# Performance work log

Measured on AMD Instinct MI355X. Metric: run time of the kernel, lower is better.

Reference implementation:

```python
import jax, jax.numpy as jnp
import numpy as np

N_HEAD = 32
D_MODEL = 4096
N_KV_GROUPS = 8
D_HEAD = D_MODEL // N_HEAD            # 128
H_PER_G = N_HEAD // N_KV_GROUPS       # 4
KV_DIM = N_KV_GROUPS * D_HEAD         # 1024
B, S = 2, 2048


def setup_inputs() -> dict:
    key = jax.random.key(0)
    ks = jax.random.split(key, 8)
    q = jax.random.normal(ks[0], (B, S, D_MODEL), dtype=jnp.float32)
    k = jax.random.normal(ks[1], (B, S, D_MODEL), dtype=jnp.float32)
    v = jax.random.normal(ks[2], (B, S, D_MODEL), dtype=jnp.float32)
    # causal mask (True = keep), broadcast over b, g, h as in the torch module
    mask = jnp.tril(jnp.ones((S, S), dtype=bool))
    # params: torch init is torch.rand (uniform [0,1)); scale down for numerics
    w_q = jax.random.uniform(ks[3], (D_MODEL, D_MODEL), dtype=jnp.float32) * 0.02
    w_k = jax.random.uniform(ks[4], (KV_DIM, D_MODEL), dtype=jnp.float32) * 0.02
    w_v = jax.random.uniform(ks[5], (KV_DIM, D_MODEL), dtype=jnp.float32) * 0.02
    w_out = jax.random.uniform(ks[6], (D_MODEL, D_MODEL), dtype=jnp.float32) * 0.02
    return {"q": q, "k": k, "v": v, "w_q": w_q, "w_k": w_k, "w_v": w_v,
            "w_out": w_out, "mask": mask}


def reference(q, k, v, w_q, w_k, w_v, w_out, mask):
    b, n, _ = q.shape
    s = k.shape[1]
    # F.linear(x, W) == x @ W.T
    query = q @ w_q.T                                  # [b, n, d_model]
    key = k @ w_k.T                                    # [b, s, kv_dim]
    value = v @ w_v.T                                  # [b, s, kv_dim]
    # b n (h d) -> b h n d -> b g h n d
    query = query.reshape(b, n, N_HEAD, D_HEAD).transpose(0, 2, 1, 3)
    query = query.reshape(b, N_KV_GROUPS, H_PER_G, n, D_HEAD)
    # b s (g d) -> b g s d
    key = key.reshape(b, s, N_KV_GROUPS, D_HEAD).transpose(0, 2, 1, 3)
    value = value.reshape(b, s, N_KV_GROUPS, D_HEAD).transpose(0, 2, 1, 3)
    scores = jnp.einsum('bghnd,bgsd->bghns', query, key) / (D_HEAD ** 0.5)
    scores = jnp.where(mask, scores, jnp.finfo(scores.dtype).min)
    attention = jax.nn.softmax(scores, axis=-1)        # [b, g, h, n, s]
    out = jnp.einsum('bghns,bgsd->bghnd', attention, value)
    # b g h n d -> b n (g h d)
    out = out.transpose(0, 3, 1, 2, 4).reshape(b, n, D_MODEL)
    return out @ w_out.T
```

## Files before the change

### kernel.cpp

```cpp
#include <hip/hip_runtime.h>

typedef unsigned short u16;
typedef unsigned int u32;
typedef __bf16 bf16x8 __attribute__((ext_vector_type(8)));
typedef float f32x4 __attribute__((ext_vector_type(4)));
typedef u16 u16x8 __attribute__((ext_vector_type(8)));
typedef u32 u32x2 __attribute__((ext_vector_type(2)));

#define SCL2E 0.12751744898229718f

__device__ __forceinline__ u16 f2bf(float f) {
  union { float f; u32 u; } x; x.f = f;
  u32 r = x.u + 0x7fffu + ((x.u >> 16) & 1u);
  return (u16)(r >> 16);
}

__device__ __forceinline__ u32 cvt_pk_bf16(float lo, float hi) {
  u32 r;
  asm("v_cvt_pk_bf16_f32 %0, %1, %2" : "=v"(r) : "v"(lo), "v"(hi));
  return r;
}

__device__ __forceinline__ void gld16(const void* g, void* l) {
  __builtin_amdgcn_global_load_lds(
      (const __attribute__((address_space(1))) u32*)g,
      (__attribute__((address_space(3))) u32*)l, 16, 0, 0);
}

#define SBAR() __builtin_amdgcn_s_barrier()
#define WAITVM(N) do { asm volatile("s_waitcnt vmcnt(" #N ")" ::: "memory"); \
                       __builtin_amdgcn_sched_barrier(0); } while (0)

#define STG(G, R0, DST, RIT, KT, K) do { \
    int rit_ = (RIT) + w*8 + lr; \
    int ch_ = lch ^ (rit_ & 7); \
    gld16((G) + ((R0) + rit_) * (long)(K) + (long)(KT)*64 + ch_*8, \
          (DST) + ((RIT) + w*8)*64); } while (0)

__device__ __forceinline__ void cvt_body(const float* __restrict__ in,
                                         u16* __restrict__ out, int n8) {
  int stride = gridDim.x * 256;
  for (int i = blockIdx.x * 256 + threadIdx.x; i < n8; i += stride) {
    float4 a = ((const float4*)in)[2*i];
    float4 b = ((const float4*)in)[2*i+1];
    u16x8 o;
    o[0]=f2bf(a.x); o[1]=f2bf(a.y); o[2]=f2bf(a.z); o[3]=f2bf(a.w);
    o[4]=f2bf(b.x); o[5]=f2bf(b.y); o[6]=f2bf(b.z); o[7]=f2bf(b.w);
    ((u16x8*)out)[i] = o;
  }
}

__global__ __launch_bounds__(256) void cvt3(
    const float* __restrict__ i0, const float* __restrict__ i1,
    const float* __restrict__ i2, u16* __restrict__ o0,
    u16* __restrict__ o1, u16* __restrict__ o2, int n8) {
  const float* in = blockIdx.y == 0 ? i0 : (blockIdx.y == 1 ? i1 : i2);
  u16* out = blockIdx.y == 0 ? o0 : (blockIdx.y == 1 ? o1 : o2);
  cvt_body(in, out, n8);
}

#define MFMA_(A, B, C) __builtin_amdgcn_mfma_f32_16x16x32_bf16(A, B, C, 0, 0, 0)

template<int OUTF32>
__device__ __forceinline__ void gemm256_body(
    const u16* __restrict__ Ag, const u16* __restrict__ Bg, void* __restrict__ Cp,
    const int K, const int ldc, const long m0, const long n0, const long cb,
    const float escale, u16* __restrict__ As, u16* __restrict__ Bs) {
  const int lane = threadIdx.x & 63, w = threadIdx.x >> 6;
  const int wm = w >> 2, wn = w & 3;
  const int c = lane & 15, grp = lane >> 4;
  const int lr = lane >> 3, lch = lane & 7;

  f32x4 acc[8][4] = {};
  const int NK = K >> 6;

  STG(Bg, n0, Bs, 0, 0, K);   STG(Bg, n0, Bs, 64, 0, K);
  STG(Bg, n0, Bs, 128, 0, K); STG(Bg, n0, Bs, 192, 0, K);
  STG(Ag, m0, As, 0, 0, K);   STG(Ag, m0, As, 128, 0, K);
  STG(Ag, m0, As, 64, 0, K);  STG(Ag, m0, As, 192, 0, K);
  {
    u16* B1 = Bs + 16384;
    STG(Bg, n0, B1, 0, 1, K);   STG(Bg, n0, B1, 64, 1, K);
    STG(Bg, n0, B1, 128, 1, K); STG(Bg, n0, B1, 192, 1, K);
  }
  WAITVM(6);
  SBAR();

  for (int kt = 0; kt < NK; ++kt) {
    const u16* At = As + (kt & 1) * 16384;
    u16* An = As + ((kt & 1) ^ 1) * 16384;
    const u16* Bt = Bs + (kt % 3) * 16384;
    u16* Bn = Bs + ((kt + 2) % 3) * 16384;
    const bool am = (kt + 1 < NK), bm = (kt + 2 < NK);

    bf16x8 bfr[4];
#define LDAF(mi, ks) (*(const bf16x8*)(At + (wm*128 + (mi)*16 + c)*64 + ((((ks)*4 + grp)) ^ (c & 7))*8))
#define LDBF(ni, ks) (*(const bf16x8*)(Bt + (wn*64  + (ni)*16 + c)*64 + ((((ks)*4 + grp)) ^ (c & 7))*8))
#define BLD(KS) bfr[0] = LDBF(0, KS); bfr[1] = LDBF(1, KS); \
                bfr[2] = LDBF(2, KS); bfr[3] = LDBF(3, KS);

#define PHASE4(MB, KS, BLOADS, STAGES, WAITS) { \
    bf16x8 a0 = LDAF((MB)+0, KS), a1 = LDAF((MB)+1, KS); \
    bf16x8 a2 = LDAF((MB)+2, KS), a3 = LDAF((MB)+3, KS); \
    BLOADS \
    STAGES \
    WAITS \
    SBAR(); \
    __builtin_amdgcn_s_setprio(1); \
    _Pragma("unroll") \
    for (int ni = 0; ni < 4; ++ni) { \
      acc[(MB)+0][ni] = MFMA_(a0, bfr[ni], acc[(MB)+0][ni]); \
      acc[(MB)+1][ni] = MFMA_(a1, bfr[ni], acc[(MB)+1][ni]); \
      acc[(MB)+2][ni] = MFMA_(a2, bfr[ni], acc[(MB)+2][ni]); \
      acc[(MB)+3][ni] = MFMA_(a3, bfr[ni], acc[(MB)+3][ni]); \
    } \
    __builtin_amdgcn_s_setprio(0); \
    SBAR(); }

    PHASE4(0, 0, BLD(0),
           if (am) { STG(Ag, m0, An, 0, kt+1, K); STG(Ag, m0, An, 128, kt+1, K); },
           if (am) { WAITVM(6); } else { WAITVM(0); })
    PHASE4(4, 0, ;,
           if (am) { STG(Ag, m0, An, 64, kt+1, K); STG(Ag, m0, An, 192, kt+1, K); }, ;)
    PHASE4(0, 1, BLD(1),
           if (bm) { STG(Bg, n0, Bn, 0, kt+2, K); STG(Bg, n0, Bn, 64, kt+2, K); }, ;)
    PHASE4(4, 1, ;,
           if (bm) { STG(Bg, n0, Bn, 128, kt+2, K); STG(Bg, n0, Bn, 192, kt+2, K); WAITVM(6); }
           else if (am) { WAITVM(2); }, ;)
#undef PHASE4
#undef BLD
#undef LDAF
#undef LDBF
  }

  #pragma unroll
  for (int mi = 0; mi < 8; ++mi) {
    #pragma unroll
    for (int rr = 0; rr < 4; ++rr) {
      long row = m0 + wm*128 + mi*16 + grp*4 + rr;
      #pragma unroll
      for (int ni = 0; ni < 4; ++ni) {
        long col = cb + wn*64 + ni*16 + c;
        if (OUTF32) ((float*)Cp)[row*ldc + col] = acc[mi][ni][rr];
        else        ((u16*)Cp)[row*ldc + col]  = f2bf(acc[mi][ni][rr] * escale);
      }
    }
  }
}

__device__ __forceinline__ void gemm128_body(
    const u16* __restrict__ Ag, const u16* __restrict__ Bg, u16* __restrict__ Cp,
    const int K, const int ldc, const long m0, const long n0, const long cb,
    u16* __restrict__ As, u16* __restrict__ Bs) {
  const int lane = threadIdx.x & 63, w = threadIdx.x >> 6;
  const int wm = w >> 2, wn = w & 3;
  const int c = lane & 15, grp = lane >> 4;
  const int lr = lane >> 3, lch = lane & 7;

  f32x4 acc[4][4] = {};
  const int NK = K >> 6;

  STG(Bg, n0, Bs, 0, 0, K);   STG(Bg, n0, Bs, 64, 0, K);
  STG(Bg, n0, Bs, 128, 0, K); STG(Bg, n0, Bs, 192, 0, K);
  STG(Ag, m0, As, 0, 0, K);   STG(Ag, m0, As, 64, 0, K);
  {
    u16* B1 = Bs + 16384; u16* A1 = As + 8192;
    STG(Bg, n0, B1, 0, 1, K);   STG(Bg, n0, B1, 64, 1, K);
    STG(Bg, n0, B1, 128, 1, K); STG(Bg, n0, B1, 192, 1, K);
    STG(Ag, m0, A1, 0, 1, K);   STG(Ag, m0, A1, 64, 1, K);
  }
  WAITVM(6);
  SBAR();

  for (int kt = 0; kt < NK; ++kt) {
    const u16* At = As + (kt % 3) * 8192;
    const u16* Bt = Bs + (kt % 3) * 16384;
    u16* An = As + ((kt + 2) % 3) * 8192;
    u16* Bn = Bs + ((kt + 2) % 3) * 16384;
    const bool bm = (kt + 2 < NK);

    bf16x8 bfr[4];
#define LDAF(mi, ks) (*(const bf16x8*)(At + (wm*64 + (mi)*16 + c)*64 + ((((ks)*4 + grp)) ^ (c & 7))*8))
#define LDBF(ni, ks) (*(const bf16x8*)(Bt + (wn*64 + (ni)*16 + c)*64 + ((((ks)*4 + grp)) ^ (c & 7))*8))

#define PHASE2K(KS, STAGES, WAITS) { \
    bf16x8 a0 = LDAF(0, KS), a1 = LDAF(1, KS); \
    bf16x8 a2 = LDAF(2, KS), a3 = LDAF(3, KS); \
    bfr[0] = LDBF(0, KS); bfr[1] = LDBF(1, KS); \
    bfr[2] = LDBF(2, KS); bfr[3] = LDBF(3, KS); \
    STAGES \
    WAITS \
    SBAR(); \
    __builtin_amdgcn_s_setprio(1); \
    _Pragma("unroll") \
    for (int ni = 0; ni < 4; ++ni) { \
      acc[0][ni] = MFMA_(a0, bfr[ni], acc[0][ni]); \
      acc[1][ni] = MFMA_(a1, bfr[ni], acc[1][ni]); \
      acc[2][ni] = MFMA_(a2, bfr[ni], acc[2][ni]); \
      acc[3][ni] = MFMA_(a3, bfr[ni], acc[3][ni]); \
    } \
    __builtin_amdgcn_s_setprio(0); \
    SBAR(); }

    PHASE2K(0, if (bm) { STG(Bg, n0, Bn, 0, kt+2, K); STG(Bg, n0, Bn, 64, kt+2, K); }, ;)
    PHASE2K(1, if (bm) { STG(Bg, n0, Bn, 128, kt+2, K); STG(Bg, n0, Bn, 192, kt+2, K);
                         STG(Ag, m0, An, 0, kt+2, K); STG(Ag, m0, An, 64, kt+2, K); },
               if (bm) { WAITVM(6); } else { WAITVM(0); })
#undef PHASE2K
#undef LDAF
#undef LDBF
  }

  #pragma unroll
  for (int mi = 0; mi < 4; ++mi) {
    #pragma unroll
    for (int rr = 0; rr < 4; ++rr) {
      long row = m0 + wm*64 + mi*16 + grp*4 + rr;
      #pragma unroll
      for (int ni = 0; ni < 4; ++ni) {
        long col = cb + wn*64 + ni*16 + c;
        Cp[row*ldc + col] = f2bf(acc[mi][ni][rr]);
      }
    }
  }
}

__global__ __launch_bounds__(512, 2) void proj_gemm(
    const u16* __restrict__ qb, const u16* __restrict__ kb,
    const u16* __restrict__ vb, const u16* __restrict__ wqb,
    const u16* __restrict__ wkv, u16* __restrict__ Qp, u16* __restrict__ KVp) {
  __shared__ __attribute__((aligned(16))) u16 SMEM[81920];
  int wg = ((int)blockIdx.x & 7) * 32 + ((int)blockIdx.x >> 3);
  gemm256_body<0>(qb, wqb, Qp, 4096, 4096,
                  (long)(wg >> 4) * 256, (long)(wg & 15) * 256, (long)(wg & 15) * 256,
                  SCL2E, SMEM, SMEM + 32768);
  {
    int mt = wg >> 3, nt = wg & 7;
    const u16* A_ = (nt < 4) ? kb : vb;
    const u16* B_ = wkv + ((nt < 4) ? 0 : 4194304);
    long n0 = (long)(nt & 3) * 256;
    long cb = (nt < 4) ? n0 : n0 + 1024;
    gemm128_body(A_, B_, KVp, 4096, 2048, (long)mt * 128, n0, cb,
                 SMEM, SMEM + 24576);
  }
}

__global__ __launch_bounds__(512, 2) void gemm_out(
    const u16* __restrict__ A, const u16* __restrict__ Bw, float* __restrict__ C) {
  __shared__ __attribute__((aligned(16))) u16 SMEM[81920];
  int wg = ((int)blockIdx.x & 7) * 32 + ((int)blockIdx.x >> 3);
  long m0 = (long)(wg >> 4) * 256, n0 = (long)(wg & 15) * 256;
  gemm256_body<1>(A, Bw, C, 4096, 4096, m0, n0, n0, 1.f, SMEM, SMEM + 32768);
}

__global__ __launch_bounds__(256) void transpose_v(
    const u16* __restrict__ KVp, u16* __restrict__ Vt) {
  const int s0 = blockIdx.x * 64, n0 = blockIdx.y * 64, b = blockIdx.z;
  const int tid = threadIdx.x;
  __shared__ __attribute__((aligned(16))) u16 t[64*80];
  #pragma unroll
  for (int p = 0; p < 2; ++p) {
    int sl = p*32 + (tid >> 3), nl = (tid & 7) * 8;
    *(u16x8*)(t + sl*80 + nl) =
        *(const u16x8*)(KVp + (long)(b*2048 + s0 + sl)*2048 + 1024 + n0 + nl);
  }
  __syncthreads();
  #pragma unroll
  for (int p = 0; p < 2; ++p) {
    int nl = p*32 + (tid >> 3), sc = (tid & 7) * 8;
    u16x8 o;
    #pragma unroll
    for (int j = 0; j < 8; ++j) o[j] = t[(sc + j)*80 + nl];
    *(u16x8*)(Vt + (long)(b*1024 + n0 + nl)*2048 + s0 + sc) = o;
  }
}

__global__ __launch_bounds__(512, 2) void attn_fwd(
    const u16* __restrict__ Qp, const u16* __restrict__ KVp,
    const u16* __restrict__ Vt, u16* __restrict__ AO) {
  const int head = blockIdx.y, b = blockIdx.z;
  const int g = head >> 2;
  const int tid = threadIdx.x, lane = tid & 63, w = tid >> 6;
  const int c = lane & 15, grp = lane >> 4;

  __shared__ __attribute__((aligned(16))) u16 Ks[2][64*128];
  __shared__ __attribute__((aligned(16))) u16 Vts[2][128*64];
  __shared__ __attribute__((aligned(16))) u16 Ps[8][32*64];
  u16* __restrict__ pw = &Ps[w][0];

  for (int half = 0; half < 2; ++half) {
    const int qt = half ? (7 - (int)blockIdx.x) : (int)blockIdx.x;
    const int q0 = qt * 256;
    const int qw = q0 + w * 32;

    bf16x8 qf[2][4];
    #pragma unroll
    for (int h = 0; h < 2; ++h) {
      const u16* qb = Qp + (long)(b*2048 + qw + h*16 + c)*4096 + head*128 + grp*8;
      #pragma unroll
      for (int t = 0; t < 4; ++t) qf[h][t] = *(const bf16x8*)(qb + t*32);
    }

    float m_run[2] = {-1e30f, -1e30f}, l_run[2] = {0.f, 0.f};
    f32x4 oacc[2][8] = {};

    const int ntiles = 4*qt + 4;

    auto STAGE = [&](int buf, int kt) {
      const int kv0 = kt * 64;
      #pragma unroll
      for (int p = 0; p < 2; ++p) {
        int idx = p*512 + w*64 + lane;
        int krow = idx >> 4, kc = idx & 15;
        int kcs = kc ^ (krow & 7);
        gld16(KVp + (long)(b*2048 + kv0 + krow)*2048 + g*128 + kcs*8,
              &Ks[buf][(p*512 + w*64)*8]);
        int d = idx >> 3, vc = idx & 7;
        int vcs = vc ^ (d & 7);
        gld16(Vt + (long)(b*1024 + g*128 + d)*2048 + kv0 + vcs*8,
              &Vts[buf][(p*512 + w*64)*8]);
      }
    };

    if (half) __syncthreads();
    STAGE(0, 0);
    int cur = 0;
    for (int kt = 0; kt < ntiles; ++kt) {
      const int kv0 = kt * 64;
      __syncthreads();
      if (kt + 1 < ntiles) STAGE(cur ^ 1, kt + 1);

      if (kv0 <= qw + 31) {
        const u16* __restrict__ Kc = &Ks[cur][0];
        const u16* __restrict__ Vc = &Vts[cur][0];

        f32x4 sacc[2][4] = {};
        __builtin_amdgcn_s_setprio(1);
        #pragma unroll
        for (int f = 0; f < 4; ++f) {
          const int row = f*16 + c;
          #pragma unroll
          for (int t = 0; t < 4; ++t) {
            bf16x8 kf = *(const bf16x8*)(Kc + row*128 + (((t*4 + grp) ^ (c & 7)) * 8));
            sacc[0][f] = __builtin_amdgcn_mfma_f32_16x16x32_bf16(kf, qf[0][t], sacc[0][f], 0, 0, 0);
            sacc[1][f] = __builtin_amdgcn_mfma_f32_16x16x32_bf16(kf, qf[1][t], sacc[1][f], 0, 0, 0);
          }
        }
        __builtin_amdgcn_s_setprio(0);

        #pragma unroll
        for (int h = 0; h < 2; ++h) {
          const int qg = qw + h*16 + c;
          float sv[16];
          if (kv0 + 63 > qw + h*16) {
            #pragma unroll
            for (int f = 0; f < 4; ++f)
              #pragma unroll
              for (int r = 0; r < 4; ++r) {
                float x = sacc[h][f][r];
                if (kv0 + f*16 + grp*4 + r > qg) x = -1e30f;
                sv[f*4 + r] = x;
              }
          } else {
            #pragma unroll
            for (int f = 0; f < 4; ++f)
              #pragma unroll
              for (int r = 0; r < 4; ++r) sv[f*4 + r] = sacc[h][f][r];
          }
          float tm[8];
          #pragma unroll
          for (int i = 0; i < 8; ++i) tm[i] = fmaxf(sv[i], sv[i+8]);
          #pragma unroll
          for (int i = 0; i < 4; ++i) tm[i] = fmaxf(tm[i], tm[i+4]);
          float tmax = fmaxf(fmaxf(tm[0], tm[2]), fmaxf(tm[1], tm[3]));
          tmax = fmaxf(tmax, __shfl_xor(tmax, 16));
          tmax = fmaxf(tmax, __shfl_xor(tmax, 32));

          float m_new = m_run[h];
          if (!__all(tmax <= m_run[h] + 8.f)) {
            m_new = fmaxf(m_run[h], tmax);
            float corr = exp2f(m_run[h] - m_new);
            l_run[h] *= corr;
            #pragma unroll
            for (int n = 0; n < 8; ++n) oacc[h][n] *= corr;
            m_run[h] = m_new;
          }

          float tsum = 0.f;
          u32 pk[8];
          #pragma unroll
          for (int i = 0; i < 8; ++i) {
            float p0 = exp2f(sv[2*i]   - m_new);
            float p1 = exp2f(sv[2*i+1] - m_new);
            tsum += p0 + p1;
            pk[i] = cvt_pk_bf16(p0, p1);
          }
          tsum += __shfl_xor(tsum, 16);
          tsum += __shfl_xor(tsum, 32);
          l_run[h] += tsum;

          #pragma unroll
          for (int f = 0; f < 4; ++f) {
            int col = (f*16 + grp*4) ^ ((c & 7) << 3);
            u32x2 pv; pv[0] = pk[2*f]; pv[1] = pk[2*f + 1];
            *(u32x2*)(pw + (h*16 + c)*64 + col) = pv;
          }
        }

        __builtin_amdgcn_s_setprio(1);
        #pragma unroll
        for (int u = 0; u < 2; ++u) {
          const int pcol = (u*32 + grp*8) ^ ((c & 7) << 3);
          bf16x8 pf0 = *(const bf16x8*)(pw + c*64 + pcol);
          bf16x8 pf1 = *(const bf16x8*)(pw + (16 + c)*64 + pcol);
          #pragma unroll
          for (int n = 0; n < 8; ++n) {
            bf16x8 vf = *(const bf16x8*)(Vc + (n*16 + c)*64 + (((u*4 + grp) ^ (c & 7)) * 8));
            oacc[0][n] = __builtin_amdgcn_mfma_f32_16x16x32_bf16(vf, pf0, oacc[0][n], 0, 0, 0);
            oacc[1][n] = __builtin_amdgcn_mfma_f32_16x16x32_bf16(vf, pf1, oacc[1][n], 0, 0, 0);
          }
        }
        __builtin_amdgcn_s_setprio(0);
      }
      cur ^= 1;
    }

    #pragma unroll
    for (int h = 0; h < 2; ++h) {
      const float inv = 1.0f / l_run[h];
      u16* ob = AO + (long)(b*2048 + qw + h*16 + c)*4096 + head*128 + grp*4;
      #pragma unroll
      for (int n = 0; n < 8; ++n) {
        u32x2 o;
        o[0] = cvt_pk_bf16(oacc[h][n][0]*inv, oacc[h][n][1]*inv);
        o[1] = cvt_pk_bf16(oacc[h][n][2]*inv, oacc[h][n][3]*inv);
        *(u32x2*)(ob + n*16) = o;
      }
    }
  }
}

extern "C" void kernel_launch(void* const* d_in, const int* in_sizes, int n_in,
                              void* d_out, int out_size, void* d_ws, size_t ws_size,
                              hipStream_t stream) {
  const float* q   = (const float*)d_in[0];
  const float* k   = (const float*)d_in[1];
  const float* v   = (const float*)d_in[2];
  const float* w_q = (const float*)d_in[3];
  const float* w_k = (const float*)d_in[4];
  const float* w_v = (const float*)d_in[5];
  const float* w_o = (const float*)d_in[6];

  u16* ws  = (u16*)d_ws;
  u16* qb  = ws;
  u16* kb  = qb  + 16777216;
  u16* vb  = kb  + 16777216;
  u16* wqb = vb  + 16777216;
  u16* wob = wqb + 16777216;
  u16* wkv = wob + 16777216;
  u16* Qp  = wkv + 8388608;
  u16* KVp = Qp  + 16777216;
  u16* Vtr = kb;
  u16* AO  = vb;
  (void)ws_size; (void)in_sizes; (void)n_in; (void)out_size;

  dim3 blk(256);
  cvt3<<<dim3(2048,3), blk, 0, stream>>>(q, k, v, qb, kb, vb, 2097152);
  cvt3<<<dim3(2048,2), blk, 0, stream>>>(w_q, w_o, w_o, wqb, wob, wob, 2097152);
  cvt3<<<dim3(512, 2), blk, 0, stream>>>(w_k, w_v, w_v, wkv, wkv + 4194304, wkv + 4194304, 524288);

  proj_gemm<<<256, dim3(512), 0, stream>>>(qb, kb, vb, wqb, wkv, Qp, KVp);
  transpose_v<<<dim3(32,16,2), blk, 0, stream>>>(KVp, Vtr);
  attn_fwd<<<dim3(4,32,2), dim3(512), 0, stream>>>(Qp, KVp, Vtr, AO);
  gemm_out<<<256, dim3(512), 0, stream>>>(AO, wob, (float*)d_out);
}
```

Before: 537.0 us.

## Collapse per-phase barriers into one barrier per k-tile in GEMM main loops

```diff
diff --git a/kernel.cpp b/kernel.cpp
--- a/kernel.cpp
+++ b/kernel.cpp
@@ -28,6 +28,7 @@
 }
 
 #define SBAR() __builtin_amdgcn_s_barrier()
+#define SCHEDB() __builtin_amdgcn_sched_barrier(0)
 #define WAITVM(N) do { asm volatile("s_waitcnt vmcnt(" #N ")" ::: "memory"); \
                        __builtin_amdgcn_sched_barrier(0); } while (0)
 
@@ -76,14 +77,14 @@
 
   STG(Bg, n0, Bs, 0, 0, K);   STG(Bg, n0, Bs, 64, 0, K);
   STG(Bg, n0, Bs, 128, 0, K); STG(Bg, n0, Bs, 192, 0, K);
-  STG(Ag, m0, As, 0, 0, K);   STG(Ag, m0, As, 128, 0, K);
-  STG(Ag, m0, As, 64, 0, K);  STG(Ag, m0, As, 192, 0, K);
+  STG(Ag, m0, As, 0, 0, K);   STG(Ag, m0, As, 64, 0, K);
+  STG(Ag, m0, As, 128, 0, K); STG(Ag, m0, As, 192, 0, K);
   {
     u16* B1 = Bs + 16384;
     STG(Bg, n0, B1, 0, 1, K);   STG(Bg, n0, B1, 64, 1, K);
     STG(Bg, n0, B1, 128, 1, K); STG(Bg, n0, B1, 192, 1, K);
   }
-  WAITVM(6);
+  WAITVM(4);
   SBAR();
 
   for (int kt = 0; kt < NK; ++kt) {
@@ -93,19 +94,10 @@
     u16* Bn = Bs + ((kt + 2) % 3) * 16384;
     const bool am = (kt + 1 < NK), bm = (kt + 2 < NK);
 
-    bf16x8 bfr[4];
+    bf16x8 a0, a1, a2, a3, bfr[4];
 #define LDAF(mi, ks) (*(const bf16x8*)(At + (wm*128 + (mi)*16 + c)*64 + ((((ks)*4 + grp)) ^ (c & 7))*8))
 #define LDBF(ni, ks) (*(const bf16x8*)(Bt + (wn*64  + (ni)*16 + c)*64 + ((((ks)*4 + grp)) ^ (c & 7))*8))
-#define BLD(KS) bfr[0] = LDBF(0, KS); bfr[1] = LDBF(1, KS); \
-                bfr[2] = LDBF(2, KS); bfr[3] = LDBF(3, KS);
-
-#define PHASE4(MB, KS, BLOADS, STAGES, WAITS) { \
-    bf16x8 a0 = LDAF((MB)+0, KS), a1 = LDAF((MB)+1, KS); \
-    bf16x8 a2 = LDAF((MB)+2, KS), a3 = LDAF((MB)+3, KS); \
-    BLOADS \
-    STAGES \
-    WAITS \
-    SBAR(); \
+#define MFMA16(MB) do { \
     __builtin_amdgcn_s_setprio(1); \
     _Pragma("unroll") \
     for (int ni = 0; ni < 4; ++ni) { \
@@ -114,21 +106,29 @@
       acc[(MB)+2][ni] = MFMA_(a2, bfr[ni], acc[(MB)+2][ni]); \
       acc[(MB)+3][ni] = MFMA_(a3, bfr[ni], acc[(MB)+3][ni]); \
     } \
-    __builtin_amdgcn_s_setprio(0); \
-    SBAR(); }
-
-    PHASE4(0, 0, BLD(0),
-           if (am) { STG(Ag, m0, An, 0, kt+1, K); STG(Ag, m0, An, 128, kt+1, K); },
-           if (am) { WAITVM(6); } else { WAITVM(0); })
-    PHASE4(4, 0, ;,
-           if (am) { STG(Ag, m0, An, 64, kt+1, K); STG(Ag, m0, An, 192, kt+1, K); }, ;)
-    PHASE4(0, 1, BLD(1),
-           if (bm) { STG(Bg, n0, Bn, 0, kt+2, K); STG(Bg, n0, Bn, 64, kt+2, K); }, ;)
-    PHASE4(4, 1, ;,
-           if (bm) { STG(Bg, n0, Bn, 128, kt+2, K); STG(Bg, n0, Bn, 192, kt+2, K); WAITVM(6); }
-           else if (am) { WAITVM(2); }, ;)
-#undef PHASE4
-#undef BLD
+    __builtin_amdgcn_s_setprio(0); } while (0)
+
+    a0 = LDAF(0,0); a1 = LDAF(1,0); a2 = LDAF(2,0); a3 = LDAF(3,0);
+    bfr[0] = LDBF(0,0); bfr[1] = LDBF(1,0); bfr[2] = LDBF(2,0); bfr[3] = LDBF(3,0);
+    if (am) { STG(Ag, m0, An, 0, kt+1, K); STG(Ag, m0, An, 64, kt+1, K);
+              STG(Ag, m0, An, 128, kt+1, K); STG(Ag, m0, An, 192, kt+1, K); }
+    MFMA16(0);
+    SCHEDB();
+    a0 = LDAF(4,0); a1 = LDAF(5,0); a2 = LDAF(6,0); a3 = LDAF(7,0);
+    if (bm) { STG(Bg, n0, Bn, 0, kt+2, K); STG(Bg, n0, Bn, 64, kt+2, K); }
+    MFMA16(4);
+    SCHEDB();
+    a0 = LDAF(0,1); a1 = LDAF(1,1); a2 = LDAF(2,1); a3 = LDAF(3,1);
+    bfr[0] = LDBF(0,1); bfr[1] = LDBF(1,1); bfr[2] = LDBF(2,1); bfr[3] = LDBF(3,1);
+    if (bm) { STG(Bg, n0, Bn, 128, kt+2, K); STG(Bg, n0, Bn, 192, kt+2, K); }
+    MFMA16(0);
+    SCHEDB();
+    a0 = LDAF(4,1); a1 = LDAF(5,1); a2 = LDAF(6,1); a3 = LDAF(7,1);
+    MFMA16(4);
+    if (bm) { WAITVM(4); } else { WAITVM(0); }
+    SBAR();
+    SCHEDB();
+#undef MFMA16
 #undef LDAF
 #undef LDBF
   }
@@ -179,18 +179,10 @@
     u16* Bn = Bs + ((kt + 2) % 3) * 16384;
     const bool bm = (kt + 2 < NK);
 
-    bf16x8 bfr[4];
+    bf16x8 a0, a1, a2, a3, bfr[4];
 #define LDAF(mi, ks) (*(const bf16x8*)(At + (wm*64 + (mi)*16 + c)*64 + ((((ks)*4 + grp)) ^ (c & 7))*8))
 #define LDBF(ni, ks) (*(const bf16x8*)(Bt + (wn*64 + (ni)*16 + c)*64 + ((((ks)*4 + grp)) ^ (c & 7))*8))
-
-#define PHASE2K(KS, STAGES, WAITS) { \
-    bf16x8 a0 = LDAF(0, KS), a1 = LDAF(1, KS); \
-    bf16x8 a2 = LDAF(2, KS), a3 = LDAF(3, KS); \
-    bfr[0] = LDBF(0, KS); bfr[1] = LDBF(1, KS); \
-    bfr[2] = LDBF(2, KS); bfr[3] = LDBF(3, KS); \
-    STAGES \
-    WAITS \
-    SBAR(); \
+#define MFMA16K() do { \
     __builtin_amdgcn_s_setprio(1); \
     _Pragma("unroll") \
     for (int ni = 0; ni < 4; ++ni) { \
@@ -199,14 +191,22 @@
       acc[2][ni] = MFMA_(a2, bfr[ni], acc[2][ni]); \
       acc[3][ni] = MFMA_(a3, bfr[ni], acc[3][ni]); \
     } \
-    __builtin_amdgcn_s_setprio(0); \
-    SBAR(); }
-
-    PHASE2K(0, if (bm) { STG(Bg, n0, Bn, 0, kt+2, K); STG(Bg, n0, Bn, 64, kt+2, K); }, ;)
-    PHASE2K(1, if (bm) { STG(Bg, n0, Bn, 128, kt+2, K); STG(Bg, n0, Bn, 192, kt+2, K);
-                         STG(Ag, m0, An, 0, kt+2, K); STG(Ag, m0, An, 64, kt+2, K); },
-               if (bm) { WAITVM(6); } else { WAITVM(0); })
-#undef PHASE2K
+    __builtin_amdgcn_s_setprio(0); } while (0)
+
+    a0 = LDAF(0,0); a1 = LDAF(1,0); a2 = LDAF(2,0); a3 = LDAF(3,0);
+    bfr[0] = LDBF(0,0); bfr[1] = LDBF(1,0); bfr[2] = LDBF(2,0); bfr[3] = LDBF(3,0);
+    if (bm) { STG(Bg, n0, Bn, 0, kt+2, K); STG(Bg, n0, Bn, 64, kt+2, K); }
+    MFMA16K();
+    SCHEDB();
+    a0 = LDAF(0,1); a1 = LDAF(1,1); a2 = LDAF(2,1); a3 = LDAF(3,1);
+    bfr[0] = LDBF(0,1); bfr[1] = LDBF(1,1); bfr[2] = LDBF(2,1); bfr[3] = LDBF(3,1);
+    if (bm) { STG(Bg, n0, Bn, 128, kt+2, K); STG(Bg, n0, Bn, 192, kt+2, K);
+              STG(Ag, m0, An, 0, kt+2, K); STG(Ag, m0, An, 64, kt+2, K); }
+    MFMA16K();
+    if (bm) { WAITVM(6); } else { WAITVM(0); }
+    SBAR();
+    SCHEDB();
+#undef MFMA16K
 #undef LDAF
 #undef LDBF
   }
```

After: 525.3 us. 2.2% less time.
